# Optimization experiments

Measured on AMD Instinct MI355X. Metric: run time of the kernel, lower is better.

## Reference

```python
import jax, jax.numpy as jnp
import numpy as np
import math

L = 4096
D = 1280
H = 16
HD = D // H  # 80
NSEG = 4


def setup_inputs() -> dict:
    key = jax.random.key(0)
    ks = jax.random.split(key, 8)
    x = jax.random.normal(ks[0], (L, D), dtype=jnp.float32)
    cu_seqlens = jnp.array([0, 1024, 2048, 3072, 4096], dtype=jnp.int32)
    rotary_pos_emb = jax.random.uniform(ks[1], (L, HD // 2), dtype=jnp.float32) * (2 * math.pi)
    s = 1.0 / math.sqrt(D)
    W_qkv = jax.random.normal(ks[2], (3 * D, D), dtype=jnp.float32) * s
    b_qkv = jax.random.normal(ks[3], (3 * D,), dtype=jnp.float32) * 0.01
    W_proj = jax.random.normal(ks[4], (D, D), dtype=jnp.float32) * s
    b_proj = jax.random.normal(ks[5], (D,), dtype=jnp.float32) * 0.01
    return {"x": x, "cu_seqlens": cu_seqlens, "rotary_pos_emb": rotary_pos_emb,
            "W_qkv": W_qkv, "b_qkv": b_qkv, "W_proj": W_proj, "b_proj": b_proj}


def _rotary_half(t):
    t1, t2 = jnp.split(t, 2, axis=-1)
    return jnp.concatenate([-t2, t1], axis=-1)


def _apply_rope(t, freq):
    # t: (L, H, HD), freq: (L, HD/2)
    cos = jnp.concatenate([jnp.cos(freq), jnp.cos(freq)], axis=-1)[:, None, :]
    sin = jnp.concatenate([jnp.sin(freq), jnp.sin(freq)], axis=-1)[:, None, :]
    return t * cos + _rotary_half(t) * sin


def reference(x, cu_seqlens, rotary_pos_emb, W_qkv, b_qkv, W_proj, b_proj):
    seq_len = x.shape[0]
    qkv = (x @ W_qkv.T + b_qkv).reshape(seq_len, 3, H, HD)
    q, k, v = qkv[:, 0], qkv[:, 1], qkv[:, 2]  # each (L, H, HD)
    q = _apply_rope(q, rotary_pos_emb)
    k = _apply_rope(k, rotary_pos_emb)
    # scores: (H, L, L)
    scores = jnp.einsum('lhd,mhd->hlm', q, k) / math.sqrt(HD)
    # block-diagonal mask from cu_seqlens: same segment -> 0, else finfo.min
    seg = jnp.searchsorted(cu_seqlens, jnp.arange(seq_len, dtype=jnp.int32), side='right')  # (L,)
    same = seg[:, None] == seg[None, :]
    neg = jnp.finfo(scores.dtype).min
    scores = scores + jnp.where(same, jnp.array(0.0, scores.dtype), neg)[None, :, :]
    attn = jax.nn.softmax(scores.astype(jnp.float32), axis=-1).astype(q.dtype)
    out = jnp.einsum('hlm,mhd->lhd', attn, v).reshape(seq_len, D)
    return out @ W_proj.T + b_proj
```

## Files before the change

### kernel.cpp

```cpp
#include <hip/hip_runtime.h>
#include <hip/hip_bf16.h>
#include <math.h>

#define LL   4096
#define DD   1280
#define HH   16
#define HDD  80
#define QKVN (3 * DD)

typedef __attribute__((ext_vector_type(8))) short sv8;
typedef __attribute__((ext_vector_type(4))) short sv4;
typedef __attribute__((ext_vector_type(4))) float fv4;

#if __has_builtin(__builtin_amdgcn_mfma_f32_16x16x16bf16_1k)
#define MFMA16(a, b, c) __builtin_amdgcn_mfma_f32_16x16x16bf16_1k(a, b, c, 0, 0, 0)
#elif __has_builtin(__builtin_amdgcn_mfma_f32_16x16x16_bf16)
#define MFMA16(a, b, c) __builtin_amdgcn_mfma_f32_16x16x16_bf16(a, b, c, 0, 0, 0)
#else
__device__ static inline fv4 MFMA16(sv4, sv4, fv4 c) { return c; }
#endif

static __device__ __forceinline__ unsigned short f2bf(float f) {
  unsigned int u = __builtin_bit_cast(unsigned int, f);
  u += 0x7FFF + ((u >> 16) & 1);
  return (unsigned short)(u >> 16);
}
static __device__ __forceinline__ float bf2f(unsigned short b) {
  unsigned int u = ((unsigned int)b) << 16;
  return __builtin_bit_cast(float, u);
}
static __device__ __forceinline__ unsigned int cvt_pk_bf16(float lo, float hi) {
  __hip_bfloat162 h = __float22bfloat162_rn(make_float2(lo, hi));
  unsigned int u;
  __builtin_memcpy(&u, &h, 4);
  return u;
}

#define GLD_LDS(gsrc, ldst)                                                          \
  __builtin_amdgcn_global_load_lds(                                                  \
      (const __attribute__((address_space(1))) unsigned int*)(gsrc),                 \
      (__attribute__((address_space(3))) unsigned int*)(ldst), 16, 0, 0)

__global__ __launch_bounds__(256) void cast3_kernel(
    const float* __restrict__ x, const float* __restrict__ w1,
    const float* __restrict__ w2, unsigned short* __restrict__ xb,
    unsigned short* __restrict__ w1b, unsigned short* __restrict__ w2b) {
  const int n0 = LL * DD / 8, n1 = QKVN * DD / 8, n2 = DD * DD / 8;
  int i = blockIdx.x * 256 + threadIdx.x;
  const float* in; unsigned short* out; int j;
  if (i < n0)           { in = x;  out = xb;  j = i; }
  else if (i < n0 + n1) { in = w1; out = w1b; j = i - n0; }
  else if (i < n0 + n1 + n2) { in = w2; out = w2b; j = i - n0 - n1; }
  else return;
  const float4* p = (const float4*)(in + (size_t)j * 8);
  float4 v0 = p[0], v1 = p[1];
  union { sv8 v; unsigned int u[4]; } o;
  o.u[0] = cvt_pk_bf16(v0.x, v0.y);
  o.u[1] = cvt_pk_bf16(v0.z, v0.w);
  o.u[2] = cvt_pk_bf16(v1.x, v1.y);
  o.u[3] = cvt_pk_bf16(v1.z, v1.w);
  *(sv8*)(out + (size_t)j * 8) = o.v;
}

__global__ __launch_bounds__(512, 2) void gemm256_bf16_kernel(
    const unsigned short* __restrict__ A, const unsigned short* __restrict__ B,
    const float* __restrict__ bias, unsigned short* __restrict__ C,
    int M, int N, int K) {
  __shared__ __attribute__((aligned(16))) unsigned short As[3][256 * 32];
  __shared__ __attribute__((aligned(16))) unsigned short Bs[3][256 * 32];
  int tid = threadIdx.x, w = tid >> 6, lane = tid & 63;
  int g = lane >> 4, l15 = lane & 15;
  int wr = w >> 2, wc = w & 3;

  int bid = blockIdx.x;
  int wg = (bid & 7) * 30 + (bid >> 3);
  int bm = (wg / 15) * 256;
  int bn = (wg % 15) * 256;

  fv4 acc[8][4];
#pragma unroll
  for (int a = 0; a < 8; ++a)
#pragma unroll
    for (int b = 0; b < 4; ++b) acc[a][b] = (fv4){0.f, 0.f, 0.f, 0.f};

  auto STAGE = [&](int buf, int t) {
    int k0 = t * 32;
#pragma unroll
    for (int i = 0; i < 4; ++i) {
      int cid = w * 4 + i;
      int c = cid & 15;
      int row = c * 16 + (lane >> 2);
      int gsrc = (lane & 3) ^ ((row >> 1) & 3);
      const unsigned short* src = (cid < 16)
          ? A + (size_t)(bm + row) * K + k0 + gsrc * 8
          : B + (size_t)(bn + row) * K + k0 + gsrc * 8;
      unsigned short* dst = ((cid < 16) ? As[buf] : Bs[buf]) + c * 512;
      GLD_LDS(src, dst);
    }
  };

  const int NT = 40;
  int r = 0;
  STAGE(0, 0);
  STAGE(1, 1);
  for (int t = 0; t < NT; ++t) {
    if (t + 1 < NT) asm volatile("s_waitcnt vmcnt(4)" ::: "memory");
    else            asm volatile("s_waitcnt vmcnt(0)" ::: "memory");
    __builtin_amdgcn_sched_barrier(0);
    asm volatile("s_barrier" ::: "memory");
    int s2 = (r == 0) ? 2 : r - 1;
    if (t + 2 < NT) STAGE(s2, t + 2);

    const unsigned short* Ab = As[r];
    const unsigned short* Bb = Bs[r];
    sv8 af[8], bfr[4];
#pragma unroll
    for (int mt = 0; mt < 8; ++mt) {
      int row = wr * 128 + mt * 16 + l15;
      af[mt] = *(const sv8*)(Ab + row * 32 + ((g ^ ((row >> 1) & 3)) * 8));
    }
#pragma unroll
    for (int nt = 0; nt < 4; ++nt) {
      int row = wc * 64 + nt * 16 + l15;
      bfr[nt] = *(const sv8*)(Bb + row * 32 + ((g ^ ((row >> 1) & 3)) * 8));
    }
#pragma unroll
    for (int mt = 0; mt < 8; ++mt)
#pragma unroll
      for (int nt = 0; nt < 4; ++nt)
        acc[mt][nt] = __builtin_amdgcn_mfma_f32_16x16x32_bf16(af[mt], bfr[nt], acc[mt][nt], 0, 0, 0);
    r = (r == 2) ? 0 : r + 1;
  }

#pragma unroll
  for (int mt = 0; mt < 8; ++mt)
#pragma unroll
    for (int nt = 0; nt < 4; ++nt) {
      int n = bn + wc * 64 + nt * 16 + l15;
      float bv = bias[n];
#pragma unroll
      for (int rr = 0; rr < 4; ++rr) {
        int m = bm + wr * 128 + mt * 16 + 4 * g + rr;
        C[(size_t)m * N + n] = f2bf(acc[mt][nt][rr] + bv);
      }
    }
}

__global__ __launch_bounds__(256) void gemm_bf16_kernel(
    const unsigned short* __restrict__ A, const unsigned short* __restrict__ B,
    const float* __restrict__ bias, void* __restrict__ Cv,
    int M, int N, int K, int out_bf16) {
  __shared__ __attribute__((aligned(16))) unsigned short As[2][128 * 64];
  __shared__ __attribute__((aligned(16))) unsigned short Bs[2][128 * 64];
  int tid = threadIdx.x, w = tid >> 6, lane = tid & 63;
  int g = lane >> 4, l15 = lane & 15;
  int wr = w >> 1, wc = w & 1;
  int bm = blockIdx.y * 128, bn = blockIdx.x * 128;

  fv4 acc[4][4];
#pragma unroll
  for (int a = 0; a < 4; ++a)
#pragma unroll
    for (int b = 0; b < 4; ++b) acc[a][b] = (fv4){0.f, 0.f, 0.f, 0.f};

  auto STAGE = [&](int buf, int k0) {
#pragma unroll
    for (int i = 0; i < 4; ++i) {
      int c = w * 4 + i;
      int row = 8 * c + (lane >> 3);
      int cb = lane & 7;
      int gcol = k0 + ((cb ^ (row & 7)) * 8);
      GLD_LDS(A + (size_t)(bm + row) * K + gcol, As[buf] + c * 512);
      GLD_LDS(B + (size_t)(bn + row) * K + gcol, Bs[buf] + c * 512);
    }
  };

  int nt = K / 64, cur = 0;
  STAGE(0, 0);
  if (nt > 1) STAGE(1, 64);
  for (int t = 0; t < nt; ++t) {
    if (t + 1 < nt) asm volatile("s_waitcnt vmcnt(8)" ::: "memory");
    else            asm volatile("s_waitcnt vmcnt(0)" ::: "memory");
    __builtin_amdgcn_sched_barrier(0);
    asm volatile("s_barrier" ::: "memory");
    const unsigned short* Ab = As[cur];
    const unsigned short* Bb = Bs[cur];
#pragma unroll
    for (int s = 0; s < 2; ++s) {
      sv8 af[4], bf[4];
#pragma unroll
      for (int t4 = 0; t4 < 4; ++t4) {
        int ra = wr * 64 + t4 * 16 + l15;
        af[t4] = *(const sv8*)(Ab + ra * 64 + (((s * 4 + g) ^ (ra & 7)) * 8));
        int rb = wc * 64 + t4 * 16 + l15;
        bf[t4] = *(const sv8*)(Bb + rb * 64 + (((s * 4 + g) ^ (rb & 7)) * 8));
      }
#pragma unroll
      for (int mt = 0; mt < 4; ++mt)
#pragma unroll
        for (int nt2 = 0; nt2 < 4; ++nt2)
          acc[mt][nt2] = __builtin_amdgcn_mfma_f32_16x16x32_bf16(af[mt], bf[nt2], acc[mt][nt2], 0, 0, 0);
    }
    asm volatile("s_waitcnt lgkmcnt(0)" ::: "memory");
    asm volatile("s_barrier" ::: "memory");
    if (t + 2 < nt) STAGE(cur, (t + 2) * 64);
    cur ^= 1;
  }

  if (out_bf16) {
    unsigned short* C = (unsigned short*)Cv;
#pragma unroll
    for (int mt = 0; mt < 4; ++mt)
#pragma unroll
      for (int nt2 = 0; nt2 < 4; ++nt2)
#pragma unroll
        for (int r = 0; r < 4; ++r) {
          int m = bm + wr * 64 + mt * 16 + 4 * g + r;
          int n = bn + wc * 64 + nt2 * 16 + l15;
          C[(size_t)m * N + n] = f2bf(acc[mt][nt2][r] + bias[n]);
        }
  } else {
    float* C = (float*)Cv;
#pragma unroll
    for (int mt = 0; mt < 4; ++mt)
#pragma unroll
      for (int nt2 = 0; nt2 < 4; ++nt2)
#pragma unroll
        for (int r = 0; r < 4; ++r) {
          int m = bm + wr * 64 + mt * 16 + 4 * g + r;
          int n = bn + wc * 64 + nt2 * 16 + l15;
          C[(size_t)m * N + n] = acc[mt][nt2][r] + bias[n];
        }
  }
}

__global__ __launch_bounds__(192) void pack_qk_kernel(
    const unsigned short* __restrict__ qkvb, const float* __restrict__ freqs,
    unsigned short* __restrict__ Qb, unsigned short* __restrict__ Kb) {
  int l = blockIdx.x;
  __shared__ float cs[40], sn[40];
  if (threadIdx.x < 40) {
    float f = freqs[(size_t)l * 40 + threadIdx.x];
    cs[threadIdx.x] = cosf(f);
    sn[threadIdx.x] = sinf(f);
  }
  __syncthreads();
  int t = threadIdx.x;
  if (t >= 160) return;
  int which = t / 80;
  int rem   = t % 80;
  int h = rem / 5, pg = rem % 5;
  int d0 = pg * 8;
  const unsigned short* src = qkvb + (size_t)l * QKVN + which * DD + h * HDD;
  union { sv8 v; unsigned short u[8]; } A, B;
  A.v = *(const sv8*)(src + d0);
  B.v = *(const sv8*)(src + d0 + 40);
  float scale = which ? 1.0f : 0.16129822676f;
  float lo[8], hi[8];
#pragma unroll
  for (int j = 0; j < 8; ++j) {
    float c = cs[d0 + j], s = sn[d0 + j];
    float a = bf2f(A.u[j]), b = bf2f(B.u[j]);
    lo[j] = (a * c - b * s) * scale;
    hi[j] = (b * c + a * s) * scale;
  }
  union { sv8 v; unsigned int u[4]; } OL, OH;
#pragma unroll
  for (int j = 0; j < 4; ++j) {
    OL.u[j] = cvt_pk_bf16(lo[2 * j], lo[2 * j + 1]);
    OH.u[j] = cvt_pk_bf16(hi[2 * j], hi[2 * j + 1]);
  }
  unsigned short* dst = (which ? Kb : Qb) + ((size_t)h * LL + l) * HDD;
  *(sv8*)(dst + d0) = OL.v;
  *(sv8*)(dst + d0 + 40) = OH.v;
}

__global__ __launch_bounds__(256) void pack_v_kernel(
    const unsigned short* __restrict__ qkvb, unsigned short* __restrict__ Vt) {
  __shared__ unsigned short vb[HDD][66];
  int l0 = blockIdx.x * 64, h = blockIdx.y;
  for (int idx = threadIdx.x; idx < 64 * HDD; idx += 256) {
    int l = idx / HDD, d = idx % HDD;
    vb[d][l] = qkvb[(size_t)(l0 + l) * QKVN + 2 * DD + h * HDD + d];
  }
  __syncthreads();
  for (int idx = threadIdx.x; idx < 64 * HDD; idx += 256) {
    int d = idx >> 6, l = idx & 63;
    Vt[((size_t)h * HDD + d) * LL + l0 + l] = vb[d][l];
  }
}

__global__ __launch_bounds__(256) void attn_mfma_kernel(
    const unsigned short* __restrict__ Qb,
    const unsigned short* __restrict__ Kb,
    const unsigned short* __restrict__ Vt,
    const int* __restrict__ cu,
    unsigned short* __restrict__ outb) {
  __shared__ __attribute__((aligned(16))) unsigned short Ks[2][64 * HDD];
  __shared__ __attribute__((aligned(16))) unsigned short Vl[2][HDD * 64];
  int tid = threadIdx.x, w = tid >> 6, lane = tid & 63;
  int g = lane >> 4, l15 = lane & 15;

  int bid = blockIdx.x;
  int sw = (bid & 7) * 128 + (bid >> 3);
  int h = sw >> 6;
  int q0 = (sw & 63) * 64;

  int s0 = 0, s1 = LL;
#pragma unroll
  for (int i = 0; i < 4; ++i) {
    int a = cu[i], b = cu[i + 1];
    if (q0 >= a && q0 < b) { s0 = a; s1 = b; }
  }

  int qrow = q0 + w * 16 + l15;
  const unsigned short* qp = Qb + ((size_t)h * LL + qrow) * HDD;
  sv8 aq[2];
#pragma unroll
  for (int s = 0; s < 2; ++s) aq[s] = *(const sv8*)(qp + s * 32 + g * 8);
  union { sv4 v; uint2 u2; } qt;
  qt.u2 = *(const uint2*)(qp + 64 + 4 * g);

  auto STAGE = [&](int buf, int kb) {
#pragma unroll
    for (int i = 0; i < 5; ++i) {
      int cid = w + 4 * i;
      if (cid < 10) {
        int B = cid * 1024 + (lane << 4);
        int row = B / 160;
        int gran = (B % 160) >> 4;
        int sgran = (gran < 8) ? (gran ^ (row & 7)) : gran;
        GLD_LDS(Kb + ((size_t)h * LL + kb + row) * HDD + sgran * 8,
                Ks[buf] + cid * 512);
      } else {
        int c = cid - 10;
        int d = 8 * c + (lane >> 3);
        int cb = lane & 7;
        GLD_LDS(Vt + ((size_t)h * HDD + d) * LL + kb + ((cb ^ (d & 7)) * 8),
                Vl[buf] + c * 512);
      }
    }
  };

  fv4 o[5];
#pragma unroll
  for (int dt = 0; dt < 5; ++dt) o[dt] = (fv4){0.f, 0.f, 0.f, 0.f};
  float lsum = 0.f;

  int cur = 0;
  STAGE(0, s0);
  if (s0 + 64 < s1) STAGE(1, s0 + 64);
  for (int kb = s0; kb < s1; kb += 64) {
    if (kb + 64 < s1) asm volatile("s_waitcnt vmcnt(5)" ::: "memory");
    else              asm volatile("s_waitcnt vmcnt(0)" ::: "memory");
    __builtin_amdgcn_sched_barrier(0);
    asm volatile("s_barrier" ::: "memory");
    const unsigned short* Kc = Ks[cur];
    const unsigned short* Vc = Vl[cur];

    fv4 sf[4];
#pragma unroll
    for (int nt = 0; nt < 4; ++nt) sf[nt] = (fv4){0.f, 0.f, 0.f, 0.f};
#pragma unroll
    for (int s = 0; s < 2; ++s) {
#pragma unroll
      for (int nt = 0; nt < 4; ++nt) {
        int key = nt * 16 + l15;
        sv8 ak = *(const sv8*)(Kc + key * HDD + (((s * 4 + g) ^ (key & 7)) * 8));
        sf[nt] = __builtin_amdgcn_mfma_f32_16x16x32_bf16(ak, aq[s], sf[nt], 0, 0, 0);
      }
    }
#pragma unroll
    for (int nt = 0; nt < 4; ++nt) {
      int key = nt * 16 + l15;
      sv4 akt = *(const sv4*)(Kc + key * HDD + (8 + (g >> 1)) * 8 + (g & 1) * 4);
      sf[nt] = MFMA16(akt, qt.v, sf[nt]);
    }

#pragma unroll
    for (int nt = 0; nt < 4; ++nt) {
      float p0 = exp2f(sf[nt][0]);
      float p1 = exp2f(sf[nt][1]);
      float p2 = exp2f(sf[nt][2]);
      float p3 = exp2f(sf[nt][3]);
      lsum += (p0 + p1) + (p2 + p3);
      union { sv4 v; unsigned int u[2]; } pa;
      pa.u[0] = cvt_pk_bf16(p0, p1);
      pa.u[1] = cvt_pk_bf16(p2, p3);
#pragma unroll
      for (int dt = 0; dt < 5; ++dt) {
        int d = dt * 16 + l15;
        sv4 vb4 = *(const sv4*)(Vc + d * 64 + (((2 * nt + (g >> 1)) ^ (d & 7)) * 8) + (g & 1) * 4);
        o[dt] = MFMA16(pa.v, vb4, o[dt]);
      }
    }
    asm volatile("s_waitcnt lgkmcnt(0)" ::: "memory");
    asm volatile("s_barrier" ::: "memory");
    if (kb + 128 < s1) STAGE(cur, kb + 128);
    cur ^= 1;
  }

  lsum += __shfl_xor(lsum, 16);
  lsum += __shfl_xor(lsum, 32);
  float inv = 1.f / lsum;
#pragma unroll
  for (int r = 0; r < 4; ++r) {
    float invr = __shfl(inv, 4 * g + r);
    int row = q0 + w * 16 + 4 * g + r;
#pragma unroll
    for (int dt = 0; dt < 5; ++dt) {
      outb[(size_t)row * DD + h * HDD + dt * 16 + l15] = f2bf(o[dt][r] * invr);
    }
  }
}

extern "C" void kernel_launch(void* const* d_in, const int* in_sizes, int n_in,
                              void* d_out, int out_size, void* d_ws, size_t ws_size,
                              hipStream_t stream) {
  const float* x     = (const float*)d_in[0];
  const int*   cu    = (const int*)d_in[1];
  const float* rope  = (const float*)d_in[2];
  const float* Wqkv  = (const float*)d_in[3];
  const float* bqkv  = (const float*)d_in[4];
  const float* Wproj = (const float*)d_in[5];
  const float* bproj = (const float*)d_in[6];
  float* out = (float*)d_out;

  char* ws = (char*)d_ws;
  unsigned short* qkvb   = (unsigned short*)ws;
  unsigned short* attn_b = (unsigned short*)ws;
  unsigned short* xb     = (unsigned short*)(ws + 31457280);
  unsigned short* Wqkvb  = (unsigned short*)(ws + 41943040);
  unsigned short* Wprojb = (unsigned short*)(ws + 51773440);
  unsigned short* Kb     = (unsigned short*)(ws + 55050240);
  unsigned short* Vt     = (unsigned short*)(ws + 71827456);
  unsigned short* Qb     = xb;

  {
    int n8 = LL * DD / 8 + QKVN * DD / 8 + DD * DD / 8;
    cast3_kernel<<<(n8 + 255) / 256, 256, 0, stream>>>(x, Wqkv, Wproj, xb, Wqkvb, Wprojb);
  }

  gemm256_bf16_kernel<<<240, 512, 0, stream>>>(
      xb, Wqkvb, bqkv, qkvb, LL, QKVN, DD);

  pack_qk_kernel<<<LL, 192, 0, stream>>>(qkvb, rope, Qb, Kb);
  pack_v_kernel<<<dim3(LL / 64, HH), 256, 0, stream>>>(qkvb, Vt);

  attn_mfma_kernel<<<1024, 256, 0, stream>>>(Qb, Kb, Vt, cu, attn_b);

  gemm_bf16_kernel<<<dim3(DD / 128, LL / 128), 256, 0, stream>>>(
      attn_b, Wprojb, bproj, out, LL, DD, DD, 0);
}
```

Baseline: 144.5 us.

## Repack K into main/tail arrays and V into MFMA-fragment order

The pack kernels now write K as a 64-wide main array plus a separately packed 16-dim tail, and V as per-block fragment-ordered 4-element groups, so the attention kernel's LDS reads match the MFMA operand layout directly. Each LDS read for the tail and V fragments becomes one contiguous 8-byte access per lane with no XOR swizzle address math, which is meant to cut bank conflicts and index arithmetic in the inner loop. The cost is more complex pack kernels and new workspace offsets. The V pack now writes 8-byte chunks instead of 2-byte scalars.

```diff
diff --git a/kernel.cpp b/kernel.cpp
--- a/kernel.cpp
+++ b/kernel.cpp
@@ -236,7 +236,8 @@
 
 __global__ __launch_bounds__(192) void pack_qk_kernel(
     const unsigned short* __restrict__ qkvb, const float* __restrict__ freqs,
-    unsigned short* __restrict__ Qb, unsigned short* __restrict__ Kb) {
+    unsigned short* __restrict__ Qb, unsigned short* __restrict__ Kmain,
+    unsigned short* __restrict__ Ktail) {
   int l = blockIdx.x;
   __shared__ float cs[40], sn[40];
   if (threadIdx.x < 40) {
@@ -270,34 +271,56 @@
     OL.u[j] = cvt_pk_bf16(lo[2 * j], lo[2 * j + 1]);
     OH.u[j] = cvt_pk_bf16(hi[2 * j], hi[2 * j + 1]);
   }
-  unsigned short* dst = (which ? Kb : Qb) + ((size_t)h * LL + l) * HDD;
-  *(sv8*)(dst + d0) = OL.v;
-  *(sv8*)(dst + d0 + 40) = OH.v;
+  if (which == 0) {
+    unsigned short* dst = Qb + ((size_t)h * LL + l) * HDD;
+    *(sv8*)(dst + d0) = OL.v;
+    *(sv8*)(dst + d0 + 40) = OH.v;
+  } else {
+    unsigned short* km = Kmain + ((size_t)h * LL + l) * 64;
+    *(sv8*)(km + pg * 8) = OL.v;
+    int dh = d0 + 40;
+    if (dh < 64) {
+      *(sv8*)(km + dh) = OH.v;
+    } else {
+      int blk = l >> 6, key = l & 63;
+      int tg0 = (dh - 64) >> 2;
+      size_t base = (((size_t)h * 64 + blk) * 4);
+      uint2 w0 = make_uint2(OH.u[0], OH.u[1]);
+      uint2 w1 = make_uint2(OH.u[2], OH.u[3]);
+      *(uint2*)(Ktail + ((base + tg0) * 64 + key) * 4)     = w0;
+      *(uint2*)(Ktail + ((base + tg0 + 1) * 64 + key) * 4) = w1;
+    }
+  }
 }
 
 __global__ __launch_bounds__(256) void pack_v_kernel(
-    const unsigned short* __restrict__ qkvb, unsigned short* __restrict__ Vt) {
-  __shared__ unsigned short vb[HDD][66];
-  int l0 = blockIdx.x * 64, h = blockIdx.y;
+    const unsigned short* __restrict__ qkvb, unsigned short* __restrict__ Vp) {
+  __shared__ unsigned short vb[HDD][72];
+  int blk = blockIdx.x, h = blockIdx.y;
+  int l0 = blk * 64;
   for (int idx = threadIdx.x; idx < 64 * HDD; idx += 256) {
     int l = idx / HDD, d = idx % HDD;
     vb[d][l] = qkvb[(size_t)(l0 + l) * QKVN + 2 * DD + h * HDD + d];
   }
   __syncthreads();
-  for (int idx = threadIdx.x; idx < 64 * HDD; idx += 256) {
-    int d = idx >> 6, l = idx & 63;
-    Vt[((size_t)h * HDD + d) * LL + l0 + l] = vb[d][l];
+  unsigned short* dst = Vp + (((size_t)h * 64 + blk) * 1280) * 4;
+  for (int idx = threadIdx.x; idx < 16 * HDD; idx += 256) {
+    int ntg = idx / HDD, d = idx % HDD;
+    uint2 v = *(const uint2*)(&vb[d][ntg * 4]);
+    *(uint2*)(dst + ((size_t)ntg * HDD + d) * 4) = v;
   }
 }
 
 __global__ __launch_bounds__(256) void attn_mfma_kernel(
     const unsigned short* __restrict__ Qb,
-    const unsigned short* __restrict__ Kb,
-    const unsigned short* __restrict__ Vt,
+    const unsigned short* __restrict__ Kmain,
+    const unsigned short* __restrict__ Ktail,
+    const unsigned short* __restrict__ Vp,
     const int* __restrict__ cu,
     unsigned short* __restrict__ outb) {
-  __shared__ __attribute__((aligned(16))) unsigned short Ks[2][64 * HDD];
-  __shared__ __attribute__((aligned(16))) unsigned short Vl[2][HDD * 64];
+  __shared__ __attribute__((aligned(16))) unsigned short Ks[2][64 * 64];
+  __shared__ __attribute__((aligned(16))) unsigned short Kt[2][4 * 64 * 4];
+  __shared__ __attribute__((aligned(16))) unsigned short Vl[2][16 * 80 * 4];
   int tid = threadIdx.x, w = tid >> 6, lane = tid & 63;
   int g = lane >> 4, l15 = lane & 15;
 
@@ -322,22 +345,23 @@
   qt.u2 = *(const uint2*)(qp + 64 + 4 * g);
 
   auto STAGE = [&](int buf, int kb) {
+    int blk = kb >> 6;
 #pragma unroll
     for (int i = 0; i < 5; ++i) {
       int cid = w + 4 * i;
-      if (cid < 10) {
-        int B = cid * 1024 + (lane << 4);
-        int row = B / 160;
-        int gran = (B % 160) >> 4;
-        int sgran = (gran < 8) ? (gran ^ (row & 7)) : gran;
-        GLD_LDS(Kb + ((size_t)h * LL + kb + row) * HDD + sgran * 8,
+      if (cid < 8) {
+        int row = 8 * cid + (lane >> 3);
+        int cb = lane & 7;
+        GLD_LDS(Kmain + ((size_t)h * LL + kb + row) * 64 + ((cb ^ (row & 7)) * 8),
                 Ks[buf] + cid * 512);
+      } else if (cid < 10) {
+        int tc = cid - 8;
+        GLD_LDS(Ktail + ((((size_t)h * 64 + blk) * 256) + tc * 128 + 2 * lane) * 4,
+                Kt[buf] + tc * 512);
       } else {
-        int c = cid - 10;
-        int d = 8 * c + (lane >> 3);
-        int cb = lane & 7;
-        GLD_LDS(Vt + ((size_t)h * HDD + d) * LL + kb + ((cb ^ (d & 7)) * 8),
-                Vl[buf] + c * 512);
+        int vc = cid - 10;
+        GLD_LDS(Vp + ((((size_t)h * 64 + blk) * 1280) + vc * 128 + 2 * lane) * 4,
+                Vl[buf] + vc * 512);
       }
     }
   };
@@ -356,6 +380,7 @@
     __builtin_amdgcn_sched_barrier(0);
     asm volatile("s_barrier" ::: "memory");
     const unsigned short* Kc = Ks[cur];
+    const unsigned short* Ktc = Kt[cur];
     const unsigned short* Vc = Vl[cur];
 
     fv4 sf[4];
@@ -366,14 +391,13 @@
 #pragma unroll
       for (int nt = 0; nt < 4; ++nt) {
         int key = nt * 16 + l15;
-        sv8 ak = *(const sv8*)(Kc + key * HDD + (((s * 4 + g) ^ (key & 7)) * 8));
+        sv8 ak = *(const sv8*)(Kc + key * 64 + (((s * 4 + g) ^ (key & 7)) * 8));
         sf[nt] = __builtin_amdgcn_mfma_f32_16x16x32_bf16(ak, aq[s], sf[nt], 0, 0, 0);
       }
     }
 #pragma unroll
     for (int nt = 0; nt < 4; ++nt) {
-      int key = nt * 16 + l15;
-      sv4 akt = *(const sv4*)(Kc + key * HDD + (8 + (g >> 1)) * 8 + (g & 1) * 4);
+      sv4 akt = *(const sv4*)(Ktc + (g * 64 + nt * 16 + l15) * 4);
       sf[nt] = MFMA16(akt, qt.v, sf[nt]);
     }
 
@@ -389,8 +413,7 @@
       pa.u[1] = cvt_pk_bf16(p2, p3);
 #pragma unroll
       for (int dt = 0; dt < 5; ++dt) {
-        int d = dt * 16 + l15;
-        sv4 vb4 = *(const sv4*)(Vc + d * 64 + (((2 * nt + (g >> 1)) ^ (d & 7)) * 8) + (g & 1) * 4);
+        sv4 vb4 = *(const sv4*)(Vc + ((nt * 4 + g) * 80 + dt * 16 + l15) * 4);
         o[dt] = MFMA16(pa.v, vb4, o[dt]);
       }
     }
@@ -432,8 +455,9 @@
   unsigned short* xb     = (unsigned short*)(ws + 31457280);
   unsigned short* Wqkvb  = (unsigned short*)(ws + 41943040);
   unsigned short* Wprojb = (unsigned short*)(ws + 51773440);
-  unsigned short* Kb     = (unsigned short*)(ws + 55050240);
-  unsigned short* Vt     = (unsigned short*)(ws + 71827456);
+  unsigned short* Kmain  = (unsigned short*)(ws + 55050240);
+  unsigned short* Ktail  = (unsigned short*)(ws + 63438848);
+  unsigned short* Vp     = (unsigned short*)(ws + 65536000);
   unsigned short* Qb     = xb;
 
   {
@@ -444,10 +468,10 @@
   gemm256_bf16_kernel<<<240, 512, 0, stream>>>(
       xb, Wqkvb, bqkv, qkvb, LL, QKVN, DD);
 
-  pack_qk_kernel<<<LL, 192, 0, stream>>>(qkvb, rope, Qb, Kb);
-  pack_v_kernel<<<dim3(LL / 64, HH), 256, 0, stream>>>(qkvb, Vt);
-
-  attn_mfma_kernel<<<1024, 256, 0, stream>>>(Qb, Kb, Vt, cu, attn_b);
+  pack_qk_kernel<<<LL, 192, 0, stream>>>(qkvb, rope, Qb, Kmain, Ktail);
+  pack_v_kernel<<<dim3(LL / 64, HH), 256, 0, stream>>>(qkvb, Vp);
+
+  attn_mfma_kernel<<<1024, 256, 0, stream>>>(Qb, Kmain, Ktail, Vp, cu, attn_b);
 
   gemm_bf16_kernel<<<dim3(DD / 128, LL / 128), 256, 0, stream>>>(
       attn_b, Wprojb, bproj, out, LL, DD, DD, 0);
```

Result: no change. 144.1 us (-0.3%).
